# Kernel tuning notes

Measured on AMD Instinct MI355X. Metric: run time of the kernel, lower is better.

## Reference

```python
import math
import jax, jax.numpy as jnp
import numpy as np

D_MODEL, N_HEADS, D_HEAD, D_INNER = 512, 8, 64, 2048
QLEN, MLEN, BATCH = 2048, 2048, 2


def _layernorm(x, g, b, eps=1e-5):
    mu = jnp.mean(x, axis=-1, keepdims=True)
    var = jnp.var(x, axis=-1, keepdims=True)
    return (x - mu) * jax.lax.rsqrt(var + eps) * g + b


def _rel_shift(x):
    # x: [qlen, klen, B, n] -> Transformer-XL relative shift
    q, k, b, n = x.shape
    x = jnp.pad(x, ((0, 0), (1, 0), (0, 0), (0, 0)))  # zero-pad key dim at front
    x = x.reshape(k + 1, q, b, n)[1:].reshape(q, k, b, n)
    return x


def setup_inputs() -> dict:
    key = jax.random.key(0)
    ks = jax.random.split(key, 16)
    nd = N_HEADS * D_HEAD
    s = 0.02
    return {
        "x": jax.random.normal(ks[0], (QLEN, BATCH, D_MODEL), jnp.float32),
        "r": jax.random.normal(ks[1], (QLEN + MLEN, D_MODEL), jnp.float32),
        "u": jax.random.normal(ks[2], (N_HEADS, D_HEAD), jnp.float32) * s,
        "v": jax.random.normal(ks[3], (N_HEADS, D_HEAD), jnp.float32) * s,
        "mems": jax.random.normal(ks[4], (MLEN, BATCH, D_MODEL), jnp.float32),
        "Wqkv": jax.random.normal(ks[5], (3 * nd, D_MODEL), jnp.float32) * s,
        "Wr": jax.random.normal(ks[6], (nd, D_MODEL), jnp.float32) * s,
        "Wo": jax.random.normal(ks[7], (D_MODEL, nd), jnp.float32) * s,
        "ln1_g": jnp.ones((D_MODEL,), jnp.float32),
        "ln1_b": jnp.zeros((D_MODEL,), jnp.float32),
        "W1": jax.random.normal(ks[8], (D_MODEL, D_INNER), jnp.float32) * s,
        "b1": jnp.zeros((D_INNER,), jnp.float32),
        "W2": jax.random.normal(ks[9], (D_INNER, D_MODEL), jnp.float32) * s,
        "b2": jnp.zeros((D_MODEL,), jnp.float32),
        "ln2_g": jnp.ones((D_MODEL,), jnp.float32),
        "ln2_b": jnp.zeros((D_MODEL,), jnp.float32),
    }


def reference(x, r, u, v, mems, Wqkv, Wr, Wo, ln1_g, ln1_b, W1, b1, W2, b2, ln2_g, ln2_b):
    qlen, B, d_model = x.shape
    n_heads, d_head = u.shape
    cat = jnp.concatenate([mems, x], axis=0)          # [klen, B, d_model]
    klen = cat.shape[0]
    mlen = klen - qlen

    qkv = cat @ Wqkv.T                                 # [klen, B, 3*n*d]
    q, k, val = jnp.split(qkv, 3, axis=-1)
    q = q[-qlen:].reshape(qlen, B, n_heads, d_head)
    k = k.reshape(klen, B, n_heads, d_head)
    val = val.reshape(klen, B, n_heads, d_head)
    rk = (r @ Wr.T).reshape(klen, n_heads, d_head)     # relative key heads

    AC = jnp.einsum('ibnd,jbnd->ijbn', q + u, k)       # content score
    BD = _rel_shift(jnp.einsum('ibnd,jnd->ijbn', q + v, rk))  # position score
    score = (AC + BD) * (1.0 / math.sqrt(d_head))      # [qlen, klen, B, n]

    # causal mask with memory: query i attends keys j <= i + mlen
    mask = jnp.arange(klen)[None, :] > (jnp.arange(qlen)[:, None] + mlen)
    score = jnp.where(mask[:, :, None, None], jnp.float32(-1e30), score)
    attn = jax.nn.softmax(score, axis=1)

    out = jnp.einsum('ijbn,jbnd->ibnd', attn, val).reshape(qlen, B, n_heads * d_head)
    out = out @ Wo.T
    h = _layernorm(x + out, ln1_g, ln1_b)              # post-LN attention

    core = jax.nn.relu(h @ W1 + b1) @ W2 + b2          # PositionwiseFF
    return _layernorm(h + core, ln2_g, ln2_b)
```

## Files before the change

kernel.cpp:

```cpp
#include <hip/hip_runtime.h>
#include <hip/hip_bf16.h>

#define QLEN 2048
#define MLEN 2048
#define KLEN 4096
#define BATCH 2
#define DMODEL 512
#define NHEADS 8
#define DHEAD 64
#define DINNER 2048

typedef __attribute__((ext_vector_type(8))) short  vs8;
typedef __attribute__((ext_vector_type(8))) __bf16 vbf8;
typedef __attribute__((ext_vector_type(4))) float  vf4;

__device__ __forceinline__ float bf2f(ushort h) {
    union { unsigned u; float f; } c; c.u = ((unsigned)h) << 16; return c.f;
}
__device__ __forceinline__ ushort f2bf(float f) {
    return __builtin_bit_cast(unsigned short, (__bf16)f);
}
__device__ __forceinline__ vf4 mfma16(vs8 a, vs8 b, vf4 c) {
    return __builtin_amdgcn_mfma_f32_16x16x32_bf16(
        __builtin_bit_cast(vbf8, a), __builtin_bit_cast(vbf8, b), c, 0, 0, 0);
}
__device__ __forceinline__ void gl16(const ushort* g, ushort* l) {
    __builtin_amdgcn_global_load_lds(
        (const __attribute__((address_space(1))) void*)g,
        (__attribute__((address_space(3))) void*)l, 16, 0, 0);
}
#define WAITV4 asm volatile("s_waitcnt vmcnt(4)" ::: "memory")
#define WAITV0 asm volatile("s_waitcnt vmcnt(0)" ::: "memory")
__device__ __forceinline__ void barx() {
    asm volatile("" ::: "memory");
    __builtin_amdgcn_s_barrier();
    asm volatile("" ::: "memory");
}

__global__ void cvt_bf(const float* __restrict__ in, ushort* __restrict__ out, int nel4) {
    int i = blockIdx.x * 256 + threadIdx.x;
    if (i < nel4) {
        float4 f = ((const float4*)in)[i];
        ushort4 o; o.x = f2bf(f.x); o.y = f2bf(f.y); o.z = f2bf(f.z); o.w = f2bf(f.w);
        ((ushort4*)out)[i] = o;
    }
}

__global__ void cvt_cat(const float* __restrict__ mems, const float* __restrict__ x,
                        ushort* __restrict__ out) {
    int i = blockIdx.x * 256 + threadIdx.x;
    const int half4 = MLEN * BATCH * DMODEL / 4;
    if (i < 2 * half4) {
        float4 f = (i < half4) ? ((const float4*)mems)[i] : ((const float4*)x)[i - half4];
        ushort4 o; o.x = f2bf(f.x); o.y = f2bf(f.y); o.z = f2bf(f.z); o.w = f2bf(f.w);
        ((ushort4*)out)[i] = o;
    }
}

__global__ void cvt_tr(const float* __restrict__ in, ushort* __restrict__ out, int R, int C) {
    __shared__ float t[32][33];
    const int c0 = blockIdx.x * 32, r0 = blockIdx.y * 32;
    const int tx = threadIdx.x & 31, ty = threadIdx.x >> 5;
#pragma unroll
    for (int q = 0; q < 4; ++q) {
        int r = ty + q * 8;
        t[r][tx] = in[(size_t)(r0 + r) * C + c0 + tx];
    }
    __syncthreads();
#pragma unroll
    for (int q = 0; q < 4; ++q) {
        int c = ty + q * 8;
        out[(size_t)(c0 + c) * R + r0 + tx] = f2bf(t[tx][c]);
    }
}

__global__ void vtrans(const ushort* __restrict__ qkv, ushort* __restrict__ vT) {
    __shared__ __align__(16) ushort t_lds[64][72];
    const int j0 = blockIdx.x * 64, n = blockIdx.y, b = blockIdx.z;
    const int tid = threadIdx.x;
#pragma unroll
    for (int p = 0; p < 2; ++p) {
        int u2 = p * 256 + tid;
        int j = u2 >> 3, d8 = (u2 & 7) * 8;
        vs8 v8 = *(const vs8*)(qkv + ((size_t)(j0 + j) * BATCH + b) * 1536 + 1024 + n * 64 + d8);
#pragma unroll
        for (int e = 0; e < 8; ++e) t_lds[d8 + e][j] = (ushort)v8[e];
    }
    __syncthreads();
#pragma unroll
    for (int p = 0; p < 2; ++p) {
        int u2 = p * 256 + tid;
        int d = u2 >> 3, j8 = (u2 & 7) * 8;
        vs8 o8 = *(const vs8*)&t_lds[d][j8];
        *(vs8*)(vT + ((size_t)(b * NHEADS + n) * 64 + d) * KLEN + j0 + j8) = o8;
    }
}

template <int EPI>
__global__ __launch_bounds__(256)
void gemm_bt(const ushort* __restrict__ A, const ushort* __restrict__ B,
             void* __restrict__ C0, void* __restrict__ C1,
             const float* __restrict__ bias, int M, int N, int K, int kc) {
    __shared__ __align__(16) ushort As[2][128 * 32];
    __shared__ __align__(16) ushort Bs[2][128 * 32];
    const int n0 = blockIdx.x * 128;
    const int m0 = blockIdx.y * 128;
    const int kb = blockIdx.z * kc;
    void* C = blockIdx.z ? C1 : C0;
    const int tid = threadIdx.x;
    const int lane = tid & 63, wave = tid >> 6;
    const int wr = wave >> 1, wc = wave & 1;
    const int lr = lane & 15, lg = lane >> 4;
    vf4 acc[4][4] = {};

    auto stage = [&](int bi, int k0) {
#pragma unroll
        for (int t = 0; t < 2; ++t) {
            int u = t * 256 + tid;
            int row = u >> 2, cu = u & 3;
            int sc = cu ^ ((row >> 1) & 3);
            gl16(&A[(size_t)(m0 + row) * K + k0 + sc * 8],
                 &As[bi][t * 2048 + (tid & 192) * 8]);
            gl16(&B[(size_t)(n0 + row) * K + k0 + sc * 8],
                 &Bs[bi][t * 2048 + (tid & 192) * 8]);
        }
    };

    const int nt = kc >> 5;
    stage(0, kb);
    int cur = 0;
    for (int t = 0; t < nt; ++t) {
        if (t + 1 < nt) { stage(cur ^ 1, kb + (t + 1) * 32); WAITV4; }
        else { WAITV0; }
        barx();
        vs8 af[4], bfr[4];
#pragma unroll
        for (int m = 0; m < 4; ++m) {
            int rr = wr * 64 + m * 16 + lr;
            af[m] = *(const vs8*)&As[cur][rr * 32 + (lg ^ ((rr >> 1) & 3)) * 8];
        }
#pragma unroll
        for (int nn = 0; nn < 4; ++nn) {
            int rr = wc * 64 + nn * 16 + lr;
            bfr[nn] = *(const vs8*)&Bs[cur][rr * 32 + (lg ^ ((rr >> 1) & 3)) * 8];
        }
#pragma unroll
        for (int m = 0; m < 4; ++m)
#pragma unroll
            for (int nn = 0; nn < 4; ++nn)
                acc[m][nn] = mfma16(af[m], bfr[nn], acc[m][nn]);
        barx();
        cur ^= 1;
    }

#pragma unroll
    for (int m = 0; m < 4; ++m) {
#pragma unroll
        for (int nn = 0; nn < 4; ++nn) {
            int row0 = m0 + wr * 64 + m * 16 + lg * 4;
            int col  = n0 + wc * 64 + nn * 16 + lr;
#pragma unroll
            for (int rr = 0; rr < 4; ++rr) {
                float vv = acc[m][nn][rr];
                size_t off = (size_t)(row0 + rr) * N + col;
                if (EPI == 0) ((float*)C)[off] = vv;
                else if (EPI == 1) ((ushort*)C)[off] = f2bf(vv);
                else if (EPI == 2) {
                    float t2 = vv + bias[col];
                    ((ushort*)C)[off] = f2bf(t2 > 0.f ? t2 : 0.f);
                } else {
                    ((ushort*)C)[(((size_t)(col >> 6)) << 18) + (size_t)(row0 + rr) * 64 + (col & 63)]
                        = f2bf(vv);
                }
            }
        }
    }
}

__global__ __launch_bounds__(256, 3)
void attn2(const ushort* __restrict__ qkv, const ushort* __restrict__ rkh,
           const ushort* __restrict__ vT, const float* __restrict__ uu,
           const float* __restrict__ vv, float* __restrict__ part_l,
           float* __restrict__ part_o) {
    __shared__ __align__(16) ushort K_lds[2][64 * 64];
    __shared__ __align__(16) ushort V_lds[2][64 * 64];
    __shared__ __align__(16) ushort w_lds[4][16 * 84];
    __shared__ __align__(16) ushort p_lds[4][16 * 72];

    const int chunk = blockIdx.x & 1, qb = blockIdx.x >> 1;
    const int b = blockIdx.y, n = blockIdx.z;
    const int tid = threadIdx.x, lane = tid & 63, w = tid >> 6;
    const int lr = lane & 15, lg = lane >> 4;
    const int i0w = qb * 64 + w * 16;

    ushort* wl = w_lds[w];
    ushort* pl = p_lds[w];
    const ushort* rh  = rkh + ((size_t)n << 18);
    const ushort* vTh = vT + (size_t)(b * NHEADS + n) * 64 * KLEN;

    vs8 aqu[2], aqv[2];
#pragma unroll
    for (int kk = 0; kk < 2; ++kk) {
        int d0 = kk * 32 + lg * 8;
        vs8 q8 = *(const vs8*)(qkv + ((size_t)(i0w + lr + MLEN) * BATCH + b) * 1536 + n * 64 + d0);
#pragma unroll
        for (int e = 0; e < 8; ++e) {
            float qf = bf2f((ushort)q8[e]);
            aqu[kk][e] = (short)f2bf((qf + uu[n * 64 + d0 + e]) * 0.125f);
            aqv[kk][e] = (short)f2bf((qf + vv[n * 64 + d0 + e]) * 0.125f);
        }
    }

    const vf4 zero4 = {0.f, 0.f, 0.f, 0.f};
    vf4 o[4] = {zero4, zero4, zero4, zero4};
    float l_run[4] = {0.f, 0.f, 0.f, 0.f};

    const int jstart = chunk ? 2048 : 0;
    const int niter = chunk ? (qb + 1) : 32;

    auto stagekv = [&](int bi, int j0) {
#pragma unroll
        for (int p = 0; p < 2; ++p) {
            int row = p * 32 + w * 8 + (lane >> 3);
            int g = ((lane & 7) - row) & 7;
            gl16(qkv + ((size_t)(j0 + row) * BATCH + b) * 1536 + 512 + n * 64 + g * 8,
                 &K_lds[bi][p * 2048 + w * 512]);
            gl16(vTh + (size_t)row * KLEN + j0 + g * 8,
                 &V_lds[bi][p * 2048 + w * 512]);
        }
    };

    stagekv(0, jstart);
    int cur = 0;
    for (int it = 0; it < niter; ++it) {
        const int j0 = jstart + it * 64;
        if (it + 1 < niter) { stagekv(cur ^ 1, j0 + 64); WAITV4; }
        else { WAITV0; }
        barx();

        vf4 acc_s[4] = {zero4, zero4, zero4, zero4};
#pragma unroll
        for (int q = 0; q < 4; ++q) {
            int jr = q * 16 + lr;
#pragma unroll
            for (int kk = 0; kk < 2; ++kk) {
                vs8 kb = *(const vs8*)&K_lds[cur][jr * 64 + ((kk * 4 + lg + jr) & 7) * 8];
                acc_s[q] = mfma16(aqu[kk], kb, acc_s[q]);
            }
        }
        const int mbase = j0 - i0w + 2032;
#pragma unroll
        for (int wg = 0; wg < 5; ++wg) {
            vf4 aw = zero4;
            int mrow = mbase + wg * 16 + lr;
            mrow = mrow > KLEN - 1 ? KLEN - 1 : mrow;
#pragma unroll
            for (int kk = 0; kk < 2; ++kk) {
                vs8 rb = *(const vs8*)(rh + (size_t)mrow * 64 + kk * 32 + lg * 8);
                aw = mfma16(aqv[kk], rb, aw);
            }
#pragma unroll
            for (int r = 0; r < 4; ++r)
                wl[(lg * 4 + r) * 84 + wg * 16 + lr] = f2bf(aw[r]);
        }

        const bool domask = chunk && (it == niter - 1);
        if (!domask) {
#pragma unroll
            for (int r = 0; r < 4; ++r) {
                int il = lg * 4 + r;
                float psum = 0.f;
#pragma unroll
                for (int q = 0; q < 4; ++q) {
                    int jl = q * 16 + lr;
                    float p4 = __expf(acc_s[q][r] + bf2f(wl[il * 84 + jl - il + 15]));
                    psum += p4;
                    pl[il * 72 + jl] = f2bf(p4);
                }
#pragma unroll
                for (int off = 1; off < 16; off <<= 1) psum += __shfl_xor(psum, off);
                l_run[r] += psum;
            }
        } else {
#pragma unroll
            for (int r = 0; r < 4; ++r) {
                int il = lg * 4 + r;
                float psum = 0.f;
#pragma unroll
                for (int q = 0; q < 4; ++q) {
                    int jl = q * 16 + lr;
                    float s = acc_s[q][r] + bf2f(wl[il * 84 + jl - il + 15]);
                    if (jl - il > w * 16) s = -1e30f;
                    float p4 = __expf(s);
                    psum += p4;
                    pl[il * 72 + jl] = f2bf(p4);
                }
#pragma unroll
                for (int off = 1; off < 16; off <<= 1) psum += __shfl_xor(psum, off);
                l_run[r] += psum;
            }
        }

#pragma unroll
        for (int jk = 0; jk < 2; ++jk) {
            vs8 pf = *(const vs8*)&pl[lr * 72 + jk * 32 + lg * 8];
#pragma unroll
            for (int dg = 0; dg < 4; ++dg) {
                int dr = dg * 16 + lr;
                vs8 vfr = *(const vs8*)&V_lds[cur][dr * 64 + ((jk * 4 + lg + dr) & 7) * 8];
                o[dg] = mfma16(pf, vfr, o[dg]);
            }
        }
        barx();
        cur ^= 1;
    }

#pragma unroll
    for (int r = 0; r < 4; ++r) {
        int i = i0w + lg * 4 + r;
        int pr = (i * 2 + b) * 8 + n;
        size_t base = ((size_t)chunk * 32768 + pr) * 64;
#pragma unroll
        for (int dg = 0; dg < 4; ++dg)
            part_o[base + dg * 16 + lr] = o[dg][r];
        if (lr == 0) part_l[chunk * 32768 + pr] = l_run[r];
    }
}

__global__ __launch_bounds__(256)
void combine(const float* __restrict__ part_l, const float* __restrict__ part_o,
             ushort* __restrict__ ao) {
    int t = blockIdx.x * 256 + threadIdx.x;
    int pr = t >> 4, d4 = (t & 15) * 4;
    float l = part_l[pr] + part_l[32768 + pr];
    float4 a = *(const float4*)&part_o[(size_t)pr * 64 + d4];
    float4 c = *(const float4*)&part_o[(size_t)(32768 + pr) * 64 + d4];
    float rl = 1.f / l;
    int i2b = pr >> 3, n = pr & 7;
    ushort* dst = ao + (size_t)i2b * 512 + n * 64 + d4;
    dst[0] = f2bf((a.x + c.x) * rl);
    dst[1] = f2bf((a.y + c.y) * rl);
    dst[2] = f2bf((a.z + c.z) * rl);
    dst[3] = f2bf((a.w + c.w) * rl);
}

__global__ __launch_bounds__(256)
void ln_fuse(const float* __restrict__ base, const float* __restrict__ pa,
             const float* __restrict__ pb, const float* __restrict__ bias,
             const float* __restrict__ g, const float* __restrict__ bb,
             float* __restrict__ of32, ushort* __restrict__ obf) {
    const int row = blockIdx.x * 4 + (threadIdx.x >> 6);
    const int lane = threadIdx.x & 63;
    const size_t off0 = (size_t)row * DMODEL + lane * 8;
    float vals[8];
    float s = 0.f, s2 = 0.f;
#pragma unroll
    for (int e = 0; e < 8; ++e) {
        float t = base[off0 + e] + pa[off0 + e];
        if (pb) t += pb[off0 + e];
        if (bias) t += bias[lane * 8 + e];
        vals[e] = t; s += t; s2 += t * t;
    }
#pragma unroll
    for (int o = 1; o < 64; o <<= 1) { s += __shfl_xor(s, o); s2 += __shfl_xor(s2, o); }
    const float mean = s * (1.f / DMODEL);
    const float var = s2 * (1.f / DMODEL) - mean * mean;
    const float rstd = rsqrtf(var + 1e-5f);
#pragma unroll
    for (int e = 0; e < 8; ++e) {
        int c = lane * 8 + e;
        float y = (vals[e] - mean) * rstd * g[c] + bb[c];
        if (of32) of32[(size_t)row * DMODEL + c] = y;
        if (obf)  obf[(size_t)row * DMODEL + c] = f2bf(y);
    }
}

extern "C" void kernel_launch(void* const* d_in, const int* in_sizes, int n_in,
                              void* d_out, int out_size, void* d_ws, size_t ws_size,
                              hipStream_t stream) {
    const float* x    = (const float*)d_in[0];
    const float* r    = (const float*)d_in[1];
    const float* u    = (const float*)d_in[2];
    const float* v    = (const float*)d_in[3];
    const float* mems = (const float*)d_in[4];
    const float* Wqkv = (const float*)d_in[5];
    const float* Wr   = (const float*)d_in[6];
    const float* Wo   = (const float*)d_in[7];
    const float* ln1g = (const float*)d_in[8];
    const float* ln1b = (const float*)d_in[9];
    const float* W1   = (const float*)d_in[10];
    const float* b1   = (const float*)d_in[11];
    const float* W2   = (const float*)d_in[12];
    const float* b2   = (const float*)d_in[13];
    const float* ln2g = (const float*)d_in[14];
    const float* ln2b = (const float*)d_in[15];
    float* out = (float*)d_out;

    char* p = (char*)d_ws;
    auto alloc = [&](size_t bytes) { char* q = p; p += (bytes + 255) & ~(size_t)255; return q; };
    ushort* cat_bf  = (ushort*)alloc((size_t)KLEN * BATCH * DMODEL * 2);
    ushort* wqkv_bf = (ushort*)alloc((size_t)1536 * 512 * 2);
    ushort* r_bf    = (ushort*)alloc((size_t)KLEN * 512 * 2);
    ushort* wr_bf   = (ushort*)alloc((size_t)512 * 512 * 2);
    ushort* wo_bf   = (ushort*)alloc((size_t)512 * 512 * 2);
    ushort* w1t_bf  = (ushort*)alloc((size_t)DINNER * 512 * 2);
    ushort* w2t_bf  = (ushort*)alloc((size_t)512 * DINNER * 2);
    ushort* qkv_bf  = (ushort*)alloc((size_t)KLEN * BATCH * 1536 * 2);
    ushort* rkh_bf  = (ushort*)alloc((size_t)KLEN * 512 * 2);
    ushort* vT      = (ushort*)alloc((size_t)BATCH * NHEADS * 64 * KLEN * 2);
    ushort* ao_bf   = (ushort*)alloc((size_t)QLEN * BATCH * 512 * 2);
    ushort* h_bf    = (ushort*)alloc((size_t)QLEN * BATCH * 512 * 2);
    ushort* ff1_bf  = (ushort*)alloc((size_t)QLEN * BATCH * DINNER * 2);
    float*  proj1a  = (float*)alloc((size_t)QLEN * BATCH * 512 * 4);
    float*  proj1b  = (float*)alloc((size_t)QLEN * BATCH * 512 * 4);
    float*  h_f32   = (float*)alloc((size_t)QLEN * BATCH * 512 * 4);
    float* part_l = (float*)cat_bf;
    float* part_o = (float*)ff1_bf;
    float* proj2a = proj1a;
    float* proj2b = proj1b;

    const int MROWS = QLEN * BATCH;
    const int CATROWS = KLEN * BATCH;

    cvt_cat<<<(CATROWS * DMODEL / 4 + 255) / 256, 256, 0, stream>>>(mems, x, cat_bf);
    cvt_bf<<<(KLEN * 512 / 4 + 255) / 256, 256, 0, stream>>>(r, r_bf, KLEN * 512 / 4);
    cvt_bf<<<(1536 * 512 / 4 + 255) / 256, 256, 0, stream>>>(Wqkv, wqkv_bf, 1536 * 512 / 4);
    cvt_bf<<<(512 * 512 / 4 + 255) / 256, 256, 0, stream>>>(Wr, wr_bf, 512 * 512 / 4);
    cvt_bf<<<(512 * 512 / 4 + 255) / 256, 256, 0, stream>>>(Wo, wo_bf, 512 * 512 / 4);
    cvt_tr<<<dim3(DINNER / 32, 512 / 32), 256, 0, stream>>>(W1, w1t_bf, 512, DINNER);
    cvt_tr<<<dim3(512 / 32, DINNER / 32), 256, 0, stream>>>(W2, w2t_bf, DINNER, 512);

    gemm_bt<1><<<dim3(1536 / 128, CATROWS / 128, 1), 256, 0, stream>>>(
        cat_bf, wqkv_bf, qkv_bf, nullptr, nullptr, CATROWS, 1536, 512, 512);
    gemm_bt<3><<<dim3(512 / 128, KLEN / 128, 1), 256, 0, stream>>>(
        r_bf, wr_bf, rkh_bf, nullptr, nullptr, KLEN, 512, 512, 512);

    vtrans<<<dim3(KLEN / 64, NHEADS, BATCH), 256, 0, stream>>>(qkv_bf, vT);
    attn2<<<dim3(64, BATCH, NHEADS), 256, 0, stream>>>(qkv_bf, rkh_bf, vT, u, v, part_l, part_o);
    combine<<<32768 * 16 / 256, 256, 0, stream>>>(part_l, part_o, ao_bf);

    gemm_bt<0><<<dim3(512 / 128, MROWS / 128, 2), 256, 0, stream>>>(
        ao_bf, wo_bf, proj1a, proj1b, nullptr, MROWS, 512, 512, 256);
    ln_fuse<<<MROWS / 4, 256, 0, stream>>>(x, proj1a, proj1b, nullptr, ln1g, ln1b, h_f32, h_bf);

    gemm_bt<2><<<dim3(DINNER / 128, MROWS / 128, 1), 256, 0, stream>>>(
        h_bf, w1t_bf, ff1_bf, nullptr, b1, MROWS, DINNER, 512, 512);
    gemm_bt<0><<<dim3(512 / 128, MROWS / 128, 2), 256, 0, stream>>>(
        ff1_bf, w2t_bf, proj2a, proj2b, nullptr, MROWS, 512, 2048, 1024);
    ln_fuse<<<MROWS / 4, 256, 0, stream>>>(h_f32, proj2a, proj2b, b2, ln2g, ln2b, out, nullptr);
}
```

Baseline: 367.4 us.

## Split attention into four key chunks, skip unneeded Q projection, register-staged KV

The attention kernel now splits the key range into four 1024-wide chunks instead of two, launches 128 blocks per (batch, head), orders query blocks heaviest-first, and skips chunks that lie entirely past the causal mask. K/V staging changes from double-buffered async LDS loads to register prefetch followed by a single-buffer LDS write, which frees LDS and allows raising launch bounds to 4 blocks per CU. Softmax uses exp2 with log2(e) folded into the query scale. The QKV GEMM is split so that Q is projected only for the current rows and not for the memory rows, using a new ldc parameter. The trade-offs are an extra barrier per iteration, a combine over four partials, and a reworked workspace layout.

```diff
diff --git a/kernel.cpp b/kernel.cpp
--- a/kernel.cpp
+++ b/kernel.cpp
@@ -100,7 +100,7 @@
 __global__ __launch_bounds__(256)
 void gemm_bt(const ushort* __restrict__ A, const ushort* __restrict__ B,
              void* __restrict__ C0, void* __restrict__ C1,
-             const float* __restrict__ bias, int M, int N, int K, int kc) {
+             const float* __restrict__ bias, int M, int N, int K, int kc, int ldc) {
     __shared__ __align__(16) ushort As[2][128 * 32];
     __shared__ __align__(16) ushort Bs[2][128 * 32];
     const int n0 = blockIdx.x * 128;
@@ -162,7 +162,7 @@
 #pragma unroll
             for (int rr = 0; rr < 4; ++rr) {
                 float vv = acc[m][nn][rr];
-                size_t off = (size_t)(row0 + rr) * N + col;
+                size_t off = (size_t)(row0 + rr) * ldc + col;
                 if (EPI == 0) ((float*)C)[off] = vv;
                 else if (EPI == 1) ((ushort*)C)[off] = f2bf(vv);
                 else if (EPI == 2) {
@@ -177,17 +177,17 @@
     }
 }
 
-__global__ __launch_bounds__(256, 3)
+__global__ __launch_bounds__(256, 4)
 void attn2(const ushort* __restrict__ qkv, const ushort* __restrict__ rkh,
            const ushort* __restrict__ vT, const float* __restrict__ uu,
            const float* __restrict__ vv, float* __restrict__ part_l,
            float* __restrict__ part_o) {
-    __shared__ __align__(16) ushort K_lds[2][64 * 64];
-    __shared__ __align__(16) ushort V_lds[2][64 * 64];
+    __shared__ __align__(16) ushort K_lds[64 * 64];
+    __shared__ __align__(16) ushort V_lds[64 * 64];
     __shared__ __align__(16) ushort w_lds[4][16 * 84];
     __shared__ __align__(16) ushort p_lds[4][16 * 72];
 
-    const int chunk = blockIdx.x & 1, qb = blockIdx.x >> 1;
+    const int chunk = blockIdx.x & 3, qb = 31 - (blockIdx.x >> 2);
     const int b = blockIdx.y, n = blockIdx.z;
     const int tid = threadIdx.x, lane = tid & 63, w = tid >> 6;
     const int lr = lane & 15, lg = lane >> 4;
@@ -198,6 +198,7 @@
     const ushort* rh  = rkh + ((size_t)n << 18);
     const ushort* vTh = vT + (size_t)(b * NHEADS + n) * 64 * KLEN;
 
+    const float S = 0.18033688011112042f;
     vs8 aqu[2], aqv[2];
 #pragma unroll
     for (int kk = 0; kk < 2; ++kk) {
@@ -206,8 +207,8 @@
 #pragma unroll
         for (int e = 0; e < 8; ++e) {
             float qf = bf2f((ushort)q8[e]);
-            aqu[kk][e] = (short)f2bf((qf + uu[n * 64 + d0 + e]) * 0.125f);
-            aqv[kk][e] = (short)f2bf((qf + vv[n * 64 + d0 + e]) * 0.125f);
+            aqu[kk][e] = (short)f2bf((qf + uu[n * 64 + d0 + e]) * S);
+            aqv[kk][e] = (short)f2bf((qf + vv[n * 64 + d0 + e]) * S);
         }
     }
 
@@ -215,104 +216,117 @@
     vf4 o[4] = {zero4, zero4, zero4, zero4};
     float l_run[4] = {0.f, 0.f, 0.f, 0.f};
 
-    const int jstart = chunk ? 2048 : 0;
-    const int niter = chunk ? (qb + 1) : 32;
-
-    auto stagekv = [&](int bi, int j0) {
-#pragma unroll
-        for (int p = 0; p < 2; ++p) {
-            int row = p * 32 + w * 8 + (lane >> 3);
-            int g = ((lane & 7) - row) & 7;
-            gl16(qkv + ((size_t)(j0 + row) * BATCH + b) * 1536 + 512 + n * 64 + g * 8,
-                 &K_lds[bi][p * 2048 + w * 512]);
-            gl16(vTh + (size_t)row * KLEN + j0 + g * 8,
-                 &V_lds[bi][p * 2048 + w * 512]);
+    const int jstart = chunk * 1024;
+    int avail = qb * 64 + 2111 - jstart;
+    int niter = avail < 0 ? 0 : (avail >> 6) + 1;
+    niter = niter > 16 ? 16 : niter;
+
+    const int slot = lane & 7;
+    vs8 kreg[2], vreg[2];
+    auto ldkv = [&](int j0) {
+#pragma unroll
+        for (int p2 = 0; p2 < 2; ++p2) {
+            int row = p2 * 32 + w * 8 + (lane >> 3);
+            int g = (slot - row) & 7;
+            kreg[p2] = *(const vs8*)(qkv + ((size_t)(j0 + row) * BATCH + b) * 1536 + 512 + n * 64 + g * 8);
+            vreg[p2] = *(const vs8*)(vTh + (size_t)row * KLEN + j0 + g * 8);
         }
     };
-
-    stagekv(0, jstart);
-    int cur = 0;
-    for (int it = 0; it < niter; ++it) {
-        const int j0 = jstart + it * 64;
-        if (it + 1 < niter) { stagekv(cur ^ 1, j0 + 64); WAITV4; }
-        else { WAITV0; }
-        barx();
-
-        vf4 acc_s[4] = {zero4, zero4, zero4, zero4};
-#pragma unroll
-        for (int q = 0; q < 4; ++q) {
-            int jr = q * 16 + lr;
-#pragma unroll
-            for (int kk = 0; kk < 2; ++kk) {
-                vs8 kb = *(const vs8*)&K_lds[cur][jr * 64 + ((kk * 4 + lg + jr) & 7) * 8];
-                acc_s[q] = mfma16(aqu[kk], kb, acc_s[q]);
+    auto wrkv = [&]() {
+#pragma unroll
+        for (int p2 = 0; p2 < 2; ++p2) {
+            int row = p2 * 32 + w * 8 + (lane >> 3);
+            *(vs8*)&K_lds[row * 64 + slot * 8] = kreg[p2];
+            *(vs8*)&V_lds[row * 64 + slot * 8] = vreg[p2];
+        }
+    };
+
+    if (niter > 0) {
+        ldkv(jstart);
+        wrkv();
+        __syncthreads();
+        for (int it = 0; it < niter; ++it) {
+            const int j0 = jstart + it * 64;
+            const bool more = (it + 1 < niter);
+            if (more) ldkv(j0 + 64);
+
+            vf4 acc_s[4] = {zero4, zero4, zero4, zero4};
+#pragma unroll
+            for (int q = 0; q < 4; ++q) {
+                int jr = q * 16 + lr;
+#pragma unroll
+                for (int kk = 0; kk < 2; ++kk) {
+                    vs8 kb = *(const vs8*)&K_lds[jr * 64 + ((kk * 4 + lg + jr) & 7) * 8];
+                    acc_s[q] = mfma16(aqu[kk], kb, acc_s[q]);
+                }
             }
-        }
-        const int mbase = j0 - i0w + 2032;
-#pragma unroll
-        for (int wg = 0; wg < 5; ++wg) {
-            vf4 aw = zero4;
-            int mrow = mbase + wg * 16 + lr;
-            mrow = mrow > KLEN - 1 ? KLEN - 1 : mrow;
-#pragma unroll
-            for (int kk = 0; kk < 2; ++kk) {
-                vs8 rb = *(const vs8*)(rh + (size_t)mrow * 64 + kk * 32 + lg * 8);
-                aw = mfma16(aqv[kk], rb, aw);
+            const int mbase = j0 - i0w + 2032;
+#pragma unroll
+            for (int wg = 0; wg < 5; ++wg) {
+                vf4 aw = zero4;
+                int mrow = mbase + wg * 16 + lr;
+                mrow = mrow > KLEN - 1 ? KLEN - 1 : mrow;
+#pragma unroll
+                for (int kk = 0; kk < 2; ++kk) {
+                    vs8 rb = *(const vs8*)(rh + (size_t)mrow * 64 + kk * 32 + lg * 8);
+                    aw = mfma16(aqv[kk], rb, aw);
+                }
+#pragma unroll
+                for (int r = 0; r < 4; ++r)
+                    wl[(lg * 4 + r) * 84 + wg * 16 + lr] = f2bf(aw[r]);
             }
-#pragma unroll
-            for (int r = 0; r < 4; ++r)
-                wl[(lg * 4 + r) * 84 + wg * 16 + lr] = f2bf(aw[r]);
-        }
-
-        const bool domask = chunk && (it == niter - 1);
-        if (!domask) {
-#pragma unroll
-            for (int r = 0; r < 4; ++r) {
-                int il = lg * 4 + r;
-                float psum = 0.f;
-#pragma unroll
-                for (int q = 0; q < 4; ++q) {
-                    int jl = q * 16 + lr;
-                    float p4 = __expf(acc_s[q][r] + bf2f(wl[il * 84 + jl - il + 15]));
-                    psum += p4;
-                    pl[il * 72 + jl] = f2bf(p4);
-                }
-#pragma unroll
-                for (int off = 1; off < 16; off <<= 1) psum += __shfl_xor(psum, off);
-                l_run[r] += psum;
+
+            const int thr = qb * 64 + w * 16 + 2048 - j0;
+            if (thr >= 63) {
+#pragma unroll
+                for (int r = 0; r < 4; ++r) {
+                    int il = lg * 4 + r;
+                    float psum = 0.f;
+#pragma unroll
+                    for (int q = 0; q < 4; ++q) {
+                        int jl = q * 16 + lr;
+                        float p4 = __builtin_amdgcn_exp2f(
+                            acc_s[q][r] + bf2f(wl[il * 84 + jl - il + 15]));
+                        psum += p4;
+                        pl[il * 72 + jl] = f2bf(p4);
+                    }
+#pragma unroll
+                    for (int off = 1; off < 16; off <<= 1) psum += __shfl_xor(psum, off);
+                    l_run[r] += psum;
+                }
+            } else {
+#pragma unroll
+                for (int r = 0; r < 4; ++r) {
+                    int il = lg * 4 + r;
+                    float psum = 0.f;
+#pragma unroll
+                    for (int q = 0; q < 4; ++q) {
+                        int jl = q * 16 + lr;
+                        float s = acc_s[q][r] + bf2f(wl[il * 84 + jl - il + 15]);
+                        if (jl - il > thr) s = -1e30f;
+                        float p4 = __builtin_amdgcn_exp2f(s);
+                        psum += p4;
+                        pl[il * 72 + jl] = f2bf(p4);
+                    }
+#pragma unroll
+                    for (int off = 1; off < 16; off <<= 1) psum += __shfl_xor(psum, off);
+                    l_run[r] += psum;
+                }
             }
-        } else {
-#pragma unroll
-            for (int r = 0; r < 4; ++r) {
-                int il = lg * 4 + r;
-                float psum = 0.f;
-#pragma unroll
-                for (int q = 0; q < 4; ++q) {
-                    int jl = q * 16 + lr;
-                    float s = acc_s[q][r] + bf2f(wl[il * 84 + jl - il + 15]);
-                    if (jl - il > w * 16) s = -1e30f;
-                    float p4 = __expf(s);
-                    psum += p4;
-                    pl[il * 72 + jl] = f2bf(p4);
-                }
-#pragma unroll
-                for (int off = 1; off < 16; off <<= 1) psum += __shfl_xor(psum, off);
-                l_run[r] += psum;
+
+#pragma unroll
+            for (int jk = 0; jk < 2; ++jk) {
+                vs8 pf = *(const vs8*)&pl[lr * 72 + jk * 32 + lg * 8];
+#pragma unroll
+                for (int dg = 0; dg < 4; ++dg) {
+                    int dr = dg * 16 + lr;
+                    vs8 vfr = *(const vs8*)&V_lds[dr * 64 + ((jk * 4 + lg + dr) & 7) * 8];
+                    o[dg] = mfma16(pf, vfr, o[dg]);
+                }
             }
-        }
-
-#pragma unroll
-        for (int jk = 0; jk < 2; ++jk) {
-            vs8 pf = *(const vs8*)&pl[lr * 72 + jk * 32 + lg * 8];
-#pragma unroll
-            for (int dg = 0; dg < 4; ++dg) {
-                int dr = dg * 16 + lr;
-                vs8 vfr = *(const vs8*)&V_lds[cur][dr * 64 + ((jk * 4 + lg + dr) & 7) * 8];
-                o[dg] = mfma16(pf, vfr, o[dg]);
-            }
-        }
-        barx();
-        cur ^= 1;
+            __syncthreads();
+            if (more) { wrkv(); __syncthreads(); }
+        }
     }
 
 #pragma unroll
@@ -332,16 +346,21 @@
              ushort* __restrict__ ao) {
     int t = blockIdx.x * 256 + threadIdx.x;
     int pr = t >> 4, d4 = (t & 15) * 4;
-    float l = part_l[pr] + part_l[32768 + pr];
-    float4 a = *(const float4*)&part_o[(size_t)pr * 64 + d4];
-    float4 c = *(const float4*)&part_o[(size_t)(32768 + pr) * 64 + d4];
+    float l = 0.f;
+    float4 s = {0.f, 0.f, 0.f, 0.f};
+#pragma unroll
+    for (int c = 0; c < 4; ++c) {
+        l += part_l[c * 32768 + pr];
+        float4 a = *(const float4*)&part_o[((size_t)c * 32768 + pr) * 64 + d4];
+        s.x += a.x; s.y += a.y; s.z += a.z; s.w += a.w;
+    }
     float rl = 1.f / l;
     int i2b = pr >> 3, n = pr & 7;
     ushort* dst = ao + (size_t)i2b * 512 + n * 64 + d4;
-    dst[0] = f2bf((a.x + c.x) * rl);
-    dst[1] = f2bf((a.y + c.y) * rl);
-    dst[2] = f2bf((a.z + c.z) * rl);
-    dst[3] = f2bf((a.w + c.w) * rl);
+    dst[0] = f2bf(s.x * rl);
+    dst[1] = f2bf(s.y * rl);
+    dst[2] = f2bf(s.z * rl);
+    dst[3] = f2bf(s.w * rl);
 }
 
 __global__ __launch_bounds__(256)
@@ -398,6 +417,7 @@
 
     char* p = (char*)d_ws;
     auto alloc = [&](size_t bytes) { char* q = p; p += (bytes + 255) & ~(size_t)255; return q; };
+    const size_t MB84 = (size_t)QLEN * BATCH * 512 * 4;
     ushort* cat_bf  = (ushort*)alloc((size_t)KLEN * BATCH * DMODEL * 2);
     ushort* wqkv_bf = (ushort*)alloc((size_t)1536 * 512 * 2);
     ushort* r_bf    = (ushort*)alloc((size_t)KLEN * 512 * 2);
@@ -410,14 +430,15 @@
     ushort* vT      = (ushort*)alloc((size_t)BATCH * NHEADS * 64 * KLEN * 2);
     ushort* ao_bf   = (ushort*)alloc((size_t)QLEN * BATCH * 512 * 2);
     ushort* h_bf    = (ushort*)alloc((size_t)QLEN * BATCH * 512 * 2);
-    ushort* ff1_bf  = (ushort*)alloc((size_t)QLEN * BATCH * DINNER * 2);
-    float*  proj1a  = (float*)alloc((size_t)QLEN * BATCH * 512 * 4);
-    float*  proj1b  = (float*)alloc((size_t)QLEN * BATCH * 512 * 4);
-    float*  h_f32   = (float*)alloc((size_t)QLEN * BATCH * 512 * 4);
-    float* part_l = (float*)cat_bf;
-    float* part_o = (float*)ff1_bf;
-    float* proj2a = proj1a;
-    float* proj2b = proj1b;
+    float*  part_l  = (float*)alloc((size_t)4 * 32768 * 4);
+    char*   big     = alloc(5 * MB84);
+    float*  part_o  = (float*)big;
+    float*  proj1a  = (float*)big;
+    float*  proj1b  = (float*)(big + MB84);
+    float*  h_f32   = (float*)(big + 2 * MB84);
+    ushort* ff1_bf  = (ushort*)(big + 3 * MB84);
+    float*  proj2a  = proj1a;
+    float*  proj2b  = proj1b;
 
     const int MROWS = QLEN * BATCH;
     const int CATROWS = KLEN * BATCH;
@@ -430,22 +451,26 @@
     cvt_tr<<<dim3(DINNER / 32, 512 / 32), 256, 0, stream>>>(W1, w1t_bf, 512, DINNER);
     cvt_tr<<<dim3(512 / 32, DINNER / 32), 256, 0, stream>>>(W2, w2t_bf, DINNER, 512);
 
-    gemm_bt<1><<<dim3(1536 / 128, CATROWS / 128, 1), 256, 0, stream>>>(
-        cat_bf, wqkv_bf, qkv_bf, nullptr, nullptr, CATROWS, 1536, 512, 512);
+    gemm_bt<1><<<dim3(1024 / 128, CATROWS / 128, 1), 256, 0, stream>>>(
+        cat_bf, wqkv_bf + (size_t)512 * 512, qkv_bf + 512, nullptr, nullptr,
+        CATROWS, 1024, 512, 512, 1536);
+    gemm_bt<1><<<dim3(512 / 128, 4096 / 128, 1), 256, 0, stream>>>(
+        cat_bf + (size_t)4096 * 512, wqkv_bf, qkv_bf + (size_t)4096 * 1536, nullptr, nullptr,
+        4096, 512, 512, 512, 1536);
     gemm_bt<3><<<dim3(512 / 128, KLEN / 128, 1), 256, 0, stream>>>(
-        r_bf, wr_bf, rkh_bf, nullptr, nullptr, KLEN, 512, 512, 512);
+        r_bf, wr_bf, rkh_bf, nullptr, nullptr, KLEN, 512, 512, 512, 512);
 
     vtrans<<<dim3(KLEN / 64, NHEADS, BATCH), 256, 0, stream>>>(qkv_bf, vT);
-    attn2<<<dim3(64, BATCH, NHEADS), 256, 0, stream>>>(qkv_bf, rkh_bf, vT, u, v, part_l, part_o);
+    attn2<<<dim3(128, BATCH, NHEADS), 256, 0, stream>>>(qkv_bf, rkh_bf, vT, u, v, part_l, part_o);
     combine<<<32768 * 16 / 256, 256, 0, stream>>>(part_l, part_o, ao_bf);
 
     gemm_bt<0><<<dim3(512 / 128, MROWS / 128, 2), 256, 0, stream>>>(
-        ao_bf, wo_bf, proj1a, proj1b, nullptr, MROWS, 512, 512, 256);
+        ao_bf, wo_bf, proj1a, proj1b, nullptr, MROWS, 512, 512, 256, 512);
     ln_fuse<<<MROWS / 4, 256, 0, stream>>>(x, proj1a, proj1b, nullptr, ln1g, ln1b, h_f32, h_bf);
 
     gemm_bt<2><<<dim3(DINNER / 128, MROWS / 128, 1), 256, 0, stream>>>(
-        h_bf, w1t_bf, ff1_bf, nullptr, b1, MROWS, DINNER, 512, 512);
+        h_bf, w1t_bf, ff1_bf, nullptr, b1, MROWS, DINNER, 512, 512, 2048);
     gemm_bt<0><<<dim3(512 / 128, MROWS / 128, 2), 256, 0, stream>>>(
-        ff1_bf, w2t_bf, proj2a, proj2b, nullptr, MROWS, 512, 2048, 1024);
+        ff1_bf, w2t_bf, proj2a, proj2b, nullptr, MROWS, 512, 2048, 1024, 512);
     ln_fuse<<<MROWS / 4, 256, 0, stream>>>(h_f32, proj2a, proj2b, b2, ln2g, ln2b, out, nullptr);
 }
```

After: 369.4 us. No clear change (+0.5%).
